# Performance work log

Measured on AMD Instinct MI355X. Metric: run time of the kernel, lower is better.

Reference implementation:

```python
import jax, jax.numpy as jnp
import numpy as np

WIN = 7
K1, K2 = 0.01, 0.03
NP_ = WIN ** 3
COV_NORM = NP_ / (NP_ - 1)


def _box3d(x, win=WIN):
    # Separable box filter: three 1D VALID convs (same math as the dense
    for ax in range(3):
        kshape = [1, 1, 1, 1, 1]
        kshape[2 + ax] = win
        k = jnp.ones(kshape, x.dtype) / win
        x = jax.lax.conv_general_dilated(
            x, k, window_strides=(1, 1, 1), padding='VALID',
            dimension_numbers=('NCDHW', 'OIDHW', 'NCDHW'))
    return x


def setup_inputs() -> dict:
    key = jax.random.key(0)
    k1, k2 = jax.random.split(key)
    B, C, D, H, W = 4, 1, 128, 128, 128
    X = jax.random.normal(k1, (B, C, D, H, W), dtype=jnp.float32)
    Y = jax.random.normal(k2, (B, C, D, H, W), dtype=jnp.float32)
    data_range = jnp.ones((B, 1, 1, 1, 1), dtype=jnp.float32)
    return {"X": X, "Y": Y, "data_range": data_range}


def reference(X, Y, data_range):
    C1 = (K1 * data_range) ** 2
    C2 = (K2 * data_range) ** 2
    ux = _box3d(X)
    uy = _box3d(Y)
    uxx = _box3d(X * X)
    uyy = _box3d(Y * Y)
    uxy = _box3d(X * Y)
    vx = COV_NORM * (uxx - ux * ux)
    vy = COV_NORM * (uyy - uy * uy)
    vxy = COV_NORM * (uxy - ux * uy)
    A1 = 2 * ux * uy + C1
    A2 = 2 * vxy + C2
    B1 = ux ** 2 + uy ** 2 + C1
    B2 = vx + vy + C2
    S = (A1 * A2) / (B1 * B2)
    return S.mean()
```

## Files before the change

### kernel.cpp

```cpp
#include <hip/hip_runtime.h>

#define NFULL 128
#define NOUT  122
#define NBLK  1024

#define WS_Q 232
#define WS_R 16
#define HS_Q 136
#define HS_R 16
#define HS_OFF 1160
#define WAVE_LDS 1856

__device__ __forceinline__ void wsum_task(const float* __restrict__ px,
                                          const float* __restrict__ py,
                                          float* __restrict__ wsp)
{
    float xs[8], ys[8];
#pragma unroll
    for (int k = 0; k < 4; ++k) {
        float2 tx = *(const float2*)(px + 2 * k);
        float2 ty = *(const float2*)(py + 2 * k);
        xs[2 * k] = tx.x; xs[2 * k + 1] = tx.y;
        ys[2 * k] = ty.x; ys[2 * k + 1] = ty.y;
    }
    float sx = 0.f, sy = 0.f, sxx = 0.f, syy = 0.f, sxy = 0.f;
#pragma unroll
    for (int k = 0; k < 7; ++k) {
        sx += xs[k]; sy += ys[k];
        sxx = fmaf(xs[k], xs[k], sxx);
        syy = fmaf(ys[k], ys[k], syy);
        sxy = fmaf(xs[k], ys[k], sxy);
    }
    float tx2 = sx - xs[0] + xs[7];
    float ty2 = sy - ys[0] + ys[7];
    float txx = sxx - xs[0] * xs[0] + xs[7] * xs[7];
    float tyy = syy - ys[0] * ys[0] + ys[7] * ys[7];
    float txy = sxy - xs[0] * ys[0] + xs[7] * ys[7];
    *(float2*)(wsp + 0 * WS_Q) = make_float2(sx,  tx2);
    *(float2*)(wsp + 1 * WS_Q) = make_float2(sy,  ty2);
    *(float2*)(wsp + 2 * WS_Q) = make_float2(sxx, txx);
    *(float2*)(wsp + 3 * WS_Q) = make_float2(syy, tyy);
    *(float2*)(wsp + 4 * WS_Q) = make_float2(sxy, txy);
}

__global__ __launch_bounds__(256, 4)
void ssim3d_kernel(const float* __restrict__ X, const float* __restrict__ Y,
                   const float* __restrict__ DR, double* __restrict__ wsout, int mode)
{
    __shared__ __align__(16) float lds[4 * WAVE_LDS];

    const int tid  = threadIdx.x;
    const int wave = tid >> 6;
    const int lane = tid & 63;
    const int c = lane & 7;
    const int g = lane >> 3;

    int bi = blockIdx.x;
    const int bb = bi & 3;  bi >>= 2;
    const int ht = bi & 3;  bi >>= 2;
    const int wt = bi & 7;  bi >>= 3;
    const int dc = bi;

    const int hbase = ht * 32 + wave * 8;
    const int w0 = wt * 16;
    const int csize = (dc < 2) ? 16 : 15;
    const int d0 = (dc < 2) ? (dc << 4) : (32 + (dc - 2) * 15);
    const int nsl = csize + 6;

    const float dr  = DR[bb];
    const float c1s = (0.01f * dr) * (0.01f * dr) * 117649.0f;
    const float c2s = (0.03f * dr) * (0.03f * dr) * 117649.0f;
    const float tni = 1.0f / 343.0f;
    const float kkA = 2.0f * 117649.0f / 342.0f;
    const float kkB = 117649.0f / 342.0f;

    float* wsb = lds + wave * WAVE_LDS;
    float* hsb = wsb + HS_OFF;

    int grow0 = hbase + g;      if (grow0 > NFULL - 1) grow0 = NFULL - 1;
    int grow1 = hbase + g + 8;  if (grow1 > NFULL - 1) grow1 = NFULL - 1;
    const bool hasA1 = (g < 6);
    int colb = w0 + 2 * c; if (colb > NFULL - 8) colb = NFULL - 8;
    float* wsp0 = wsb + lane * 2;
    float* wsp1 = wsb + 128 + lane * 2;

    const bool actB = (lane < 40);
    const int cB = lane & 7;
    const int qB = lane >> 3;
    const float* srcB = wsb + qB * WS_Q + 2 * cB;
    float*       dstB = hsb + qB * HS_Q + 2 * cB;

    const float* srcC = hsb + lane * 2;
    const int gh  = hbase + g;
    const int gw0 = w0 + 2 * c;
    const bool vh   = (gh < NOUT);
    const bool vld0 = vh && (gw0 < NOUT);
    const bool vld1 = vh && (gw0 + 1 < NOUT);

    const size_t planeStride = (size_t)NFULL * NFULL;
    const size_t bbase = (size_t)bb * NFULL * planeStride;

    float2 ring[7][5];
    float2 run[5];
#pragma unroll
    for (int k = 0; k < 7; ++k)
#pragma unroll
        for (int q = 0; q < 5; ++q) ring[k][q] = make_float2(0.f, 0.f);
#pragma unroll
    for (int q = 0; q < 5; ++q) run[q] = make_float2(0.f, 0.f);
    float acc = 0.0f;

    for (int base = 0; base < nsl; base += 7) {
#pragma unroll
        for (int u = 0; u < 7; ++u) {
            const int s = base + u;
            if (s < nsl) {
                const int dIn = d0 + s;
                const float* Xp = X + bbase + (size_t)dIn * planeStride;
                const float* Yp = Y + bbase + (size_t)dIn * planeStride;

                wsum_task(Xp + grow0 * NFULL + colb, Yp + grow0 * NFULL + colb, wsp0);
                if (hasA1)
                    wsum_task(Xp + grow1 * NFULL + colb, Yp + grow1 * NFULL + colb, wsp1);

                if (actB) {
                    float2 v[14];
#pragma unroll
                    for (int r = 0; r < 14; ++r)
                        v[r] = *(const float2*)(srcB + r * WS_R);
                    float ax = v[0].x, ay = v[0].y;
#pragma unroll
                    for (int r = 1; r < 7; ++r) { ax += v[r].x; ay += v[r].y; }
                    *(float2*)(dstB + 0 * HS_R) = make_float2(ax, ay);
#pragma unroll
                    for (int i = 1; i < 8; ++i) {
                        ax += v[6 + i].x - v[i - 1].x;
                        ay += v[6 + i].y - v[i - 1].y;
                        *(float2*)(dstB + i * HS_R) = make_float2(ax, ay);
                    }
                }

                {
                    const int slot = u;
                    float2 p[5];
#pragma unroll
                    for (int q = 0; q < 5; ++q)
                        p[q] = *(const float2*)(srcC + q * HS_Q);
#pragma unroll
                    for (int q = 0; q < 5; ++q) {
                        run[q].x += p[q].x - ring[slot][q].x;
                        run[q].y += p[q].y - ring[slot][q].y;
                        ring[slot][q] = p[q];
                    }
                    if (s >= 6) {
#pragma unroll
                        for (int j = 0; j < 2; ++j) {
                            const bool vld = j ? vld1 : vld0;
                            if (vld) {
                                float Sx  = j ? run[0].y : run[0].x;
                                float Sy  = j ? run[1].y : run[1].x;
                                float Sxx = j ? run[2].y : run[2].x;
                                float Syy = j ? run[3].y : run[3].x;
                                float Sxy = j ? run[4].y : run[4].x;
                                float P = Sx * Sy;
                                float Q = fmaf(Sx, Sx, Sy * Sy);
                                float A1 = fmaf(2.f, P, c1s);
                                float A2 = fmaf(kkA, fmaf(-tni, P, Sxy), c2s);
                                float B1 = Q + c1s;
                                float B2 = fmaf(kkB, fmaf(-tni, Q, Sxx + Syy), c2s);
                                float num = A1 * A2;
                                float den = B1 * B2;
                                float r0 = __builtin_amdgcn_rcpf(den);
                                r0 = r0 * fmaf(-den, r0, 2.0f);
                                acc = fmaf(num, r0, acc);
                            }
                        }
                    }
                }
            }
        }
    }

#pragma unroll
    for (int off = 32; off; off >>= 1) acc += __shfl_down(acc, off);
    __syncthreads();
    if (lane == 0) lds[wave] = acc;
    __syncthreads();
    if (tid == 0) {
        double t = (double)lds[0] + (double)lds[1] + (double)lds[2] + (double)lds[3];
        if (mode) wsout[blockIdx.x] = t;
        else      atomicAdd(wsout, t);
    }
}

__global__ void ssim3d_finalize(const double* __restrict__ ws, float* __restrict__ out, int mode)
{
    if (mode) {
        __shared__ double sm[4];
        const int tid = threadIdx.x;
        double t = 0.0;
        for (int i = tid; i < NBLK; i += 256) t += ws[i];
#pragma unroll
        for (int off = 32; off; off >>= 1) t += __shfl_down(t, off);
        if ((tid & 63) == 0) sm[tid >> 6] = t;
        __syncthreads();
        if (tid == 0) {
            double r = sm[0] + sm[1] + sm[2] + sm[3];
            out[0] = (float)(r * (1.0 / 7263392.0));
        }
    } else {
        if (threadIdx.x == 0)
            out[0] = (float)(ws[0] * (1.0 / 7263392.0));
    }
}

extern "C" void kernel_launch(void* const* d_in, const int* in_sizes, int n_in,
                              void* d_out, int out_size, void* d_ws, size_t ws_size,
                              hipStream_t stream)
{
    const float* X  = (const float*)d_in[0];
    const float* Y  = (const float*)d_in[1];
    const float* DR = (const float*)d_in[2];
    double* ws = (double*)d_ws;

    const int mode = (ws_size >= NBLK * sizeof(double)) ? 1 : 0;
    if (!mode) hipMemsetAsync(d_ws, 0, sizeof(double), stream);
    ssim3d_kernel<<<NBLK, 256, 0, stream>>>(X, Y, DR, ws, mode);
    ssim3d_finalize<<<1, 256, 0, stream>>>(ws, (float*)d_out, mode);
}
```

Measured before the change: 129.3 us.

## Replace LDS H-direction box sum with DPP row-shift reductions in registers

The H-direction 7-tap sum no longer goes through a per-wave LDS staging buffer. Lanes are remapped so each 16-lane DPP row holds 16 consecutive H rows, and the sum is built from DPP row_shl adds entirely in registers. Tiling changes to 10 useful H rows per 16 lanes, 13 H tiles and 5 D chunks of about 25 slices, giving 1040 blocks. This removes the LDS traffic and its latency, at the cost of 6 of every 16 lanes doing load and W-sum work whose output is discarded, and more redundant halo loads along H.

```diff
diff --git a/kernel.cpp b/kernel.cpp
--- a/kernel.cpp
+++ b/kernel.cpp
@@ -2,69 +2,38 @@
 
 #define NFULL 128
 #define NOUT  122
-#define NBLK  1024
+#define NBLK  1040
 
-#define WS_Q 232
-#define WS_R 16
-#define HS_Q 136
-#define HS_R 16
-#define HS_OFF 1160
-#define WAVE_LDS 1856
-
-__device__ __forceinline__ void wsum_task(const float* __restrict__ px,
-                                          const float* __restrict__ py,
-                                          float* __restrict__ wsp)
-{
-    float xs[8], ys[8];
-#pragma unroll
-    for (int k = 0; k < 4; ++k) {
-        float2 tx = *(const float2*)(px + 2 * k);
-        float2 ty = *(const float2*)(py + 2 * k);
-        xs[2 * k] = tx.x; xs[2 * k + 1] = tx.y;
-        ys[2 * k] = ty.x; ys[2 * k + 1] = ty.y;
-    }
-    float sx = 0.f, sy = 0.f, sxx = 0.f, syy = 0.f, sxy = 0.f;
-#pragma unroll
-    for (int k = 0; k < 7; ++k) {
-        sx += xs[k]; sy += ys[k];
-        sxx = fmaf(xs[k], xs[k], sxx);
-        syy = fmaf(ys[k], ys[k], syy);
-        sxy = fmaf(xs[k], ys[k], sxy);
-    }
-    float tx2 = sx - xs[0] + xs[7];
-    float ty2 = sy - ys[0] + ys[7];
-    float txx = sxx - xs[0] * xs[0] + xs[7] * xs[7];
-    float tyy = syy - ys[0] * ys[0] + ys[7] * ys[7];
-    float txy = sxy - xs[0] * ys[0] + xs[7] * ys[7];
-    *(float2*)(wsp + 0 * WS_Q) = make_float2(sx,  tx2);
-    *(float2*)(wsp + 1 * WS_Q) = make_float2(sy,  ty2);
-    *(float2*)(wsp + 2 * WS_Q) = make_float2(sxx, txx);
-    *(float2*)(wsp + 3 * WS_Q) = make_float2(syy, tyy);
-    *(float2*)(wsp + 4 * WS_Q) = make_float2(sxy, txy);
+template<int CTRL>
+__device__ __forceinline__ float dppshl(float v) {
+    return __int_as_float(
+        __builtin_amdgcn_update_dpp(0, __float_as_int(v), CTRL, 0xF, 0xF, true));
 }
 
 __global__ __launch_bounds__(256, 4)
 void ssim3d_kernel(const float* __restrict__ X, const float* __restrict__ Y,
                    const float* __restrict__ DR, double* __restrict__ wsout, int mode)
 {
-    __shared__ __align__(16) float lds[4 * WAVE_LDS];
+    __shared__ float sm[4];
 
     const int tid  = threadIdx.x;
     const int wave = tid >> 6;
     const int lane = tid & 63;
-    const int c = lane & 7;
-    const int g = lane >> 3;
+    const int h = lane & 15;
+    const int c = lane >> 4;
 
     int bi = blockIdx.x;
     const int bb = bi & 3;  bi >>= 2;
-    const int ht = bi & 3;  bi >>= 2;
-    const int wt = bi & 7;  bi >>= 3;
-    const int dc = bi;
+    const int wt = bi & 3;  bi >>= 2;
+    const int ht = bi % 13;
+    const int dc = bi / 13;
 
-    const int hbase = ht * 32 + wave * 8;
-    const int w0 = wt * 16;
-    const int csize = (dc < 2) ? 16 : 15;
-    const int d0 = (dc < 2) ? (dc << 4) : (32 + (dc - 2) * 15);
+    const int hb = ht * 10;
+    int grow = hb + h; if (grow > NFULL - 1) grow = NFULL - 1;
+    const int wbase = wt * 32 + wave * 8;
+    int colb = wbase + 2 * c; if (colb > NFULL - 8) colb = NFULL - 8;
+    const int csize = (dc < 2) ? 25 : 24;
+    const int d0 = (dc < 2) ? 25 * dc : 50 + (dc - 2) * 24;
     const int nsl = csize + 6;
 
     const float dr  = DR[bb];
@@ -74,40 +43,25 @@
     const float kkA = 2.0f * 117649.0f / 342.0f;
     const float kkB = 117649.0f / 342.0f;
 
-    float* wsb = lds + wave * WAVE_LDS;
-    float* hsb = wsb + HS_OFF;
-
-    int grow0 = hbase + g;      if (grow0 > NFULL - 1) grow0 = NFULL - 1;
-    int grow1 = hbase + g + 8;  if (grow1 > NFULL - 1) grow1 = NFULL - 1;
-    const bool hasA1 = (g < 6);
-    int colb = w0 + 2 * c; if (colb > NFULL - 8) colb = NFULL - 8;
-    float* wsp0 = wsb + lane * 2;
-    float* wsp1 = wsb + 128 + lane * 2;
-
-    const bool actB = (lane < 40);
-    const int cB = lane & 7;
-    const int qB = lane >> 3;
-    const float* srcB = wsb + qB * WS_Q + 2 * cB;
-    float*       dstB = hsb + qB * HS_Q + 2 * cB;
-
-    const float* srcC = hsb + lane * 2;
-    const int gh  = hbase + g;
-    const int gw0 = w0 + 2 * c;
-    const bool vh   = (gh < NOUT);
+    const int gh  = hb + h;
+    const int gw0 = wbase + 2 * c;
+    const bool vh   = (h < 10) && (gh < NOUT);
     const bool vld0 = vh && (gw0 < NOUT);
     const bool vld1 = vh && (gw0 + 1 < NOUT);
 
     const size_t planeStride = (size_t)NFULL * NFULL;
-    const size_t bbase = (size_t)bb * NFULL * planeStride;
+    const size_t rowoff = (size_t)bb * NFULL * planeStride
+                        + (size_t)grow * NFULL + colb
+                        + (size_t)d0 * planeStride;
 
-    float2 ring[7][5];
-    float2 run[5];
+    float ring[7][10];
+    float run[10];
 #pragma unroll
     for (int k = 0; k < 7; ++k)
 #pragma unroll
-        for (int q = 0; q < 5; ++q) ring[k][q] = make_float2(0.f, 0.f);
+        for (int q = 0; q < 10; ++q) ring[k][q] = 0.f;
 #pragma unroll
-    for (int q = 0; q < 5; ++q) run[q] = make_float2(0.f, 0.f);
+    for (int q = 0; q < 10; ++q) run[q] = 0.f;
     float acc = 0.0f;
 
     for (int base = 0; base < nsl; base += 7) {
@@ -115,65 +69,67 @@
         for (int u = 0; u < 7; ++u) {
             const int s = base + u;
             if (s < nsl) {
-                const int dIn = d0 + s;
-                const float* Xp = X + bbase + (size_t)dIn * planeStride;
-                const float* Yp = Y + bbase + (size_t)dIn * planeStride;
+                const float* px = X + rowoff + (size_t)s * planeStride;
+                const float* py = Y + rowoff + (size_t)s * planeStride;
 
-                wsum_task(Xp + grow0 * NFULL + colb, Yp + grow0 * NFULL + colb, wsp0);
-                if (hasA1)
-                    wsum_task(Xp + grow1 * NFULL + colb, Yp + grow1 * NFULL + colb, wsp1);
-
-                if (actB) {
-                    float2 v[14];
+                float xs[8], ys[8];
 #pragma unroll
-                    for (int r = 0; r < 14; ++r)
-                        v[r] = *(const float2*)(srcB + r * WS_R);
-                    float ax = v[0].x, ay = v[0].y;
+                for (int k = 0; k < 4; ++k) {
+                    float2 tx = *(const float2*)(px + 2 * k);
+                    float2 ty = *(const float2*)(py + 2 * k);
+                    xs[2 * k] = tx.x; xs[2 * k + 1] = tx.y;
+                    ys[2 * k] = ty.x; ys[2 * k + 1] = ty.y;
+                }
+                float f[10];
+                {
+                    float sx = 0.f, sy = 0.f, sxx = 0.f, syy = 0.f, sxy = 0.f;
 #pragma unroll
-                    for (int r = 1; r < 7; ++r) { ax += v[r].x; ay += v[r].y; }
-                    *(float2*)(dstB + 0 * HS_R) = make_float2(ax, ay);
-#pragma unroll
-                    for (int i = 1; i < 8; ++i) {
-                        ax += v[6 + i].x - v[i - 1].x;
-                        ay += v[6 + i].y - v[i - 1].y;
-                        *(float2*)(dstB + i * HS_R) = make_float2(ax, ay);
+                    for (int k = 0; k < 7; ++k) {
+                        sx += xs[k]; sy += ys[k];
+                        sxx = fmaf(xs[k], xs[k], sxx);
+                        syy = fmaf(ys[k], ys[k], syy);
+                        sxy = fmaf(xs[k], ys[k], sxy);
                     }
+                    f[0] = sx;  f[1] = sx - xs[0] + xs[7];
+                    f[2] = sy;  f[3] = sy - ys[0] + ys[7];
+                    f[4] = sxx; f[5] = sxx - xs[0] * xs[0] + xs[7] * xs[7];
+                    f[6] = syy; f[7] = syy - ys[0] * ys[0] + ys[7] * ys[7];
+                    f[8] = sxy; f[9] = sxy - xs[0] * ys[0] + xs[7] * ys[7];
                 }
 
-                {
-                    const int slot = u;
-                    float2 p[5];
+                const int slot = u;
 #pragma unroll
-                    for (int q = 0; q < 5; ++q)
-                        p[q] = *(const float2*)(srcC + q * HS_Q);
+                for (int q = 0; q < 10; ++q) {
+                    float v  = f[q];
+                    float t1 = v  + dppshl<0x101>(v);
+                    float t2 = t1 + dppshl<0x102>(t1);
+                    float t3 = t2 + dppshl<0x104>(t1);
+                    float g  = t3 + dppshl<0x106>(v);
+                    run[q] += g - ring[slot][q];
+                    ring[slot][q] = g;
+                }
+
+                if (s >= 6) {
 #pragma unroll
-                    for (int q = 0; q < 5; ++q) {
-                        run[q].x += p[q].x - ring[slot][q].x;
-                        run[q].y += p[q].y - ring[slot][q].y;
-                        ring[slot][q] = p[q];
-                    }
-                    if (s >= 6) {
-#pragma unroll
-                        for (int j = 0; j < 2; ++j) {
-                            const bool vld = j ? vld1 : vld0;
-                            if (vld) {
-                                float Sx  = j ? run[0].y : run[0].x;
-                                float Sy  = j ? run[1].y : run[1].x;
-                                float Sxx = j ? run[2].y : run[2].x;
-                                float Syy = j ? run[3].y : run[3].x;
-                                float Sxy = j ? run[4].y : run[4].x;
-                                float P = Sx * Sy;
-                                float Q = fmaf(Sx, Sx, Sy * Sy);
-                                float A1 = fmaf(2.f, P, c1s);
-                                float A2 = fmaf(kkA, fmaf(-tni, P, Sxy), c2s);
-                                float B1 = Q + c1s;
-                                float B2 = fmaf(kkB, fmaf(-tni, Q, Sxx + Syy), c2s);
-                                float num = A1 * A2;
-                                float den = B1 * B2;
-                                float r0 = __builtin_amdgcn_rcpf(den);
-                                r0 = r0 * fmaf(-den, r0, 2.0f);
-                                acc = fmaf(num, r0, acc);
-                            }
+                    for (int j = 0; j < 2; ++j) {
+                        const bool vld = j ? vld1 : vld0;
+                        if (vld) {
+                            float Sx  = run[0 + j];
+                            float Sy  = run[2 + j];
+                            float Sxx = run[4 + j];
+                            float Syy = run[6 + j];
+                            float Sxy = run[8 + j];
+                            float P = Sx * Sy;
+                            float Q = fmaf(Sx, Sx, Sy * Sy);
+                            float A1 = fmaf(2.f, P, c1s);
+                            float A2 = fmaf(kkA, fmaf(-tni, P, Sxy), c2s);
+                            float B1 = Q + c1s;
+                            float B2 = fmaf(kkB, fmaf(-tni, Q, Sxx + Syy), c2s);
+                            float num = A1 * A2;
+                            float den = B1 * B2;
+                            float r0 = __builtin_amdgcn_rcpf(den);
+                            r0 = r0 * fmaf(-den, r0, 2.0f);
+                            acc = fmaf(num, r0, acc);
                         }
                     }
                 }
@@ -183,11 +139,10 @@
 
 #pragma unroll
     for (int off = 32; off; off >>= 1) acc += __shfl_down(acc, off);
-    __syncthreads();
-    if (lane == 0) lds[wave] = acc;
+    if (lane == 0) sm[wave] = acc;
     __syncthreads();
     if (tid == 0) {
-        double t = (double)lds[0] + (double)lds[1] + (double)lds[2] + (double)lds[3];
+        double t = (double)sm[0] + (double)sm[1] + (double)sm[2] + (double)sm[3];
         if (mode) wsout[blockIdx.x] = t;
         else      atomicAdd(wsout, t);
     }
```

After: 157.5 us. 21.8% more time.
